# Optimization experiments

Hardware: AMD Instinct MI355X
Metric: run time of the kernel (lower is better)

## Reference

```python
import math
import jax, jax.numpy as jnp
import numpy as np

B, S, HID = 2, 2048, 4096
H, KV = 32, 8
D = HID // H  # 128


def setup_inputs() -> dict:
    key = jax.random.key(0)
    ks = jax.random.split(key, 6)
    std = 0.02
    x = jax.random.normal(ks[0], (B, S, HID), dtype=jnp.float32)
    # causal additive mask, broadcast over batch and heads
    neg = jnp.full((S, S), -1e9, dtype=jnp.float32)
    mask = jnp.triu(neg, k=1)[None, None, :, :]
    q_w = jax.random.normal(ks[1], (HID, HID), dtype=jnp.float32) * std
    k_w = jax.random.normal(ks[2], (KV * D, HID), dtype=jnp.float32) * std
    v_w = jax.random.normal(ks[3], (KV * D, HID), dtype=jnp.float32) * std
    o_w = jax.random.normal(ks[4], (HID, HID), dtype=jnp.float32) * std
    return {
        "x": x, "mask": mask,
        "q_w": q_w, "q_b": jnp.zeros((HID,), jnp.float32),
        "k_w": k_w, "k_b": jnp.zeros((KV * D,), jnp.float32),
        "v_w": v_w, "v_b": jnp.zeros((KV * D,), jnp.float32),
        "o_w": o_w, "o_b": jnp.zeros((HID,), jnp.float32),
    }


def reference(x, mask, q_w, q_b, k_w, k_b, v_w, v_b, o_w, o_b):
    b, s, _ = x.shape
    rep = H // KV
    # projections (torch Linear convention: y = x @ W^T + b)
    q = (x @ q_w.T + q_b).reshape(b, s, H, D)
    k = (x @ k_w.T + k_b).reshape(b, s, KV, D)
    v = (x @ v_w.T + v_b).reshape(b, s, KV, D)
    # GQA kv-head repeat via concat: q head i attends to kv head (i mod KV)
    k = jnp.concatenate([k] * rep, axis=2)  # [b, s, H, D]
    v = jnp.concatenate([v] * rep, axis=2)
    # [b, H, s, D]
    q = q.transpose(0, 2, 1, 3)
    k = k.transpose(0, 2, 1, 3)
    v = v.transpose(0, 2, 1, 3)
    scores = jnp.einsum("bhqd,bhkd->bhqk", q, k) / math.sqrt(D)
    scores = scores + mask
    w = jax.nn.softmax(scores, axis=-1)
    attn = jnp.einsum("bhqk,bhkd->bhqd", w, v)
    attn = attn.transpose(0, 2, 1, 3).reshape(b, s, HID)
    return attn @ o_w.T + o_b
```

## Files before the change

### kernel.cpp

```cpp
#include <hip/hip_runtime.h>
#include <hip/hip_bf16.h>
#include <cstdint>

typedef __attribute__((ext_vector_type(8))) short s8vec;
typedef __attribute__((ext_vector_type(4))) float f4vec;

#define DEV __device__ __forceinline__

constexpr int Bn = 2, Sn = 2048, HIDn = 4096, Hn = 32, KVn = 8, Dn = 128;

typedef const __attribute__((address_space(1))) void gvoid_t;
typedef __attribute__((address_space(3))) void lvoid_t;

DEV void async_ld16(const void* g, void* l) {
  __builtin_amdgcn_global_load_lds((gvoid_t*)g, (lvoid_t*)l, 16, 0, 0);
}

DEV f4vec mfma16(s8vec a, s8vec b, f4vec c) {
  return __builtin_amdgcn_mfma_f32_16x16x32_bf16(a, b, c, 0, 0, 0);
}

__global__ void cvt_all(const float* __restrict__ x, const float* __restrict__ qw,
                        const float* __restrict__ kw, const float* __restrict__ vw,
                        const float* __restrict__ ow,
                        __hip_bfloat16* __restrict__ xb, __hip_bfloat16* __restrict__ qwb,
                        __hip_bfloat16* __restrict__ kwb, __hip_bfloat16* __restrict__ vwb,
                        __hip_bfloat16* __restrict__ owb) {
  const int i = blockIdx.x * 256 + threadIdx.x;
  const float* src; __hip_bfloat16* dst; int off;
  if (i < 4194304)       { src = x;  dst = xb;  off = i; }
  else if (i < 8388608)  { src = qw; dst = qwb; off = i - 4194304; }
  else if (i < 9437184)  { src = kw; dst = kwb; off = i - 8388608; }
  else if (i < 10485760) { src = vw; dst = vwb; off = i - 9437184; }
  else                   { src = ow; dst = owb; off = i - 10485760; }
  float4 f = ((const float4*)src)[off];
  union { __hip_bfloat16 h[4]; uint2 u; } cv;
  cv.h[0] = __float2bfloat16(f.x);
  cv.h[1] = __float2bfloat16(f.y);
  cv.h[2] = __float2bfloat16(f.z);
  cv.h[3] = __float2bfloat16(f.w);
  ((uint2*)dst)[off] = cv.u;
}

template <typename EpiF>
DEV void gemm_bt_body(const __hip_bfloat16* A, const __hip_bfloat16* Bw, int K,
                      long m0, long n0, EpiF epi) {
  __shared__ __hip_bfloat16 As[2][256 * 64];
  __shared__ __hip_bfloat16 Bs[2][256 * 64];
  const int t = threadIdx.x;
  const int w = t >> 6, l = t & 63;
  const int lane15 = l & 15, quad = l >> 4;
  const int wm = (w >> 2) << 7;
  const int wn = (w & 3) << 6;

  f4vec acc[8][4] = {};

  const int srow = w * 8 + (l >> 3);
  const int scol = ((l & 7) ^ (l >> 3)) << 3;
  const __hip_bfloat16* gA = A + (m0 + srow) * (long)K + scol;
  const __hip_bfloat16* gB = Bw + (n0 + srow) * (long)K + scol;
  const long i64K = (long)K << 6;

  auto stage = [&](int buf, int kt) {
    char* la = (char*)As[buf] + (w << 10);
    char* lb = (char*)Bs[buf] + (w << 10);
    const long ko = (long)kt << 6;
#pragma unroll
    for (int i = 0; i < 4; i++) async_ld16(gA + (long)i * i64K + ko, la + i * 8192);
#pragma unroll
    for (int i = 0; i < 4; i++) async_ld16(gB + (long)i * i64K + ko, lb + i * 8192);
  };

  const int arA = (wm + lane15) << 7;
  const int arB = (wn + lane15) << 7;
  const int c0 = (quad << 4) ^ ((lane15 & 7) << 4);
  const int c1 = c0 ^ 64;

  const int NT = K >> 6;

  stage(0, 0);
  stage(1, 1);
  asm volatile("s_waitcnt vmcnt(8)" ::: "memory");
  __builtin_amdgcn_s_barrier();
  __builtin_amdgcn_sched_barrier(0);

  for (int tau = 0; tau < NT; ++tau) {
    const int cur = tau & 1;
    const char* Ab = (const char*)As[cur];
    const char* Bb = (const char*)Bs[cur];
    s8vec af0[8], af1[8], bf0[4], bf1[4];
#pragma unroll
    for (int i = 0; i < 8; i++) {
      af0[i] = *(const s8vec*)(Ab + arA + i * 2048 + c0);
      af1[i] = *(const s8vec*)(Ab + arA + i * 2048 + c1);
    }
#pragma unroll
    for (int j = 0; j < 4; j++) {
      bf0[j] = *(const s8vec*)(Bb + arB + j * 2048 + c0);
      bf1[j] = *(const s8vec*)(Bb + arB + j * 2048 + c1);
    }
    __builtin_amdgcn_s_setprio(1);
#pragma unroll
    for (int i = 0; i < 8; i++)
#pragma unroll
      for (int j = 0; j < 4; j++) acc[i][j] = mfma16(af0[i], bf0[j], acc[i][j]);
    __builtin_amdgcn_s_setprio(0);
    __builtin_amdgcn_sched_barrier(0);
    asm volatile("s_waitcnt lgkmcnt(0)" ::: "memory");
    __builtin_amdgcn_sched_barrier(0);
    __builtin_amdgcn_s_barrier();
    if (tau + 2 < NT) stage(cur, tau + 2);
    __builtin_amdgcn_s_setprio(1);
#pragma unroll
    for (int i = 0; i < 8; i++)
#pragma unroll
      for (int j = 0; j < 4; j++) acc[i][j] = mfma16(af1[i], bf1[j], acc[i][j]);
    __builtin_amdgcn_s_setprio(0);
    if (tau + 1 < NT) {
      if (tau + 2 < NT) asm volatile("s_waitcnt vmcnt(8)" ::: "memory");
      else              asm volatile("s_waitcnt vmcnt(0)" ::: "memory");
      __builtin_amdgcn_s_barrier();
      __builtin_amdgcn_sched_barrier(0);
    }
  }
  epi(acc, wm, wn, lane15, quad);
}

__launch_bounds__(512, 1)
__global__ void gemm_qkv(const __hip_bfloat16* __restrict__ xb,
                         const __hip_bfloat16* __restrict__ qwb,
                         const __hip_bfloat16* __restrict__ kwb,
                         const __hip_bfloat16* __restrict__ vwb,
                         const float* __restrict__ qb, const float* __restrict__ kb,
                         const float* __restrict__ vb,
                         __hip_bfloat16* __restrict__ qh, __hip_bfloat16* __restrict__ kh,
                         __hip_bfloat16* __restrict__ vth) {
  const int bx = blockIdx.x;
  const long m0 = (long)blockIdx.y << 8;
  int mode; long n0;
  const __hip_bfloat16* Bw; const float* bias;
  if (bx < 16)      { mode = 0; Bw = qwb; bias = qb; n0 = (long)bx << 8; }
  else if (bx < 20) { mode = 1; Bw = kwb; bias = kb; n0 = (long)(bx - 16) << 8; }
  else              { mode = 2; Bw = vwb; bias = vb; n0 = (long)(bx - 20) << 8; }

  gemm_bt_body(xb, Bw, 4096, m0, n0,
    [&](f4vec (&acc)[8][4], int wm, int wn, int lane15, int quad) {
      float bv[4];
#pragma unroll
      for (int j = 0; j < 4; j++) bv[j] = bias[n0 + wn + j * 16 + lane15];
#pragma unroll
      for (int i = 0; i < 8; i++)
#pragma unroll
        for (int j = 0; j < 4; j++)
#pragma unroll
          for (int r = 0; r < 4; r++) {
            const long gm = m0 + wm + i * 16 + (quad << 2) + r;
            const long gn = n0 + wn + j * 16 + lane15;
            const float v = acc[i][j][r] + bv[j];
            const long bb = gm >> 11, ss = gm & 2047;
            const long hh = gn >> 7, dd = gn & 127;
            const __hip_bfloat16 hv = __float2bfloat16(v);
            if (mode == 0)
              qh[(((bb * Hn + hh) * Sn + ss) << 7) + dd] = hv;
            else if (mode == 1)
              kh[(((bb * KVn + hh) * Sn + ss) << 7) + dd] = hv;
            else
              vth[((bb * KVn + hh) * Dn + dd) * (long)Sn + ss] = hv;
          }
    });
}

__launch_bounds__(512, 1)
__global__ void gemm_out(const __hip_bfloat16* __restrict__ A,
                         const __hip_bfloat16* __restrict__ Bw,
                         const float* __restrict__ bias, float* __restrict__ Cout) {
  const long m0 = (long)blockIdx.y << 8;
  const long n0 = (long)blockIdx.x << 8;
  gemm_bt_body(A, Bw, 4096, m0, n0,
    [&](f4vec (&acc)[8][4], int wm, int wn, int lane15, int quad) {
      float bv[4];
#pragma unroll
      for (int j = 0; j < 4; j++) bv[j] = bias[n0 + wn + j * 16 + lane15];
#pragma unroll
      for (int i = 0; i < 8; i++)
#pragma unroll
        for (int j = 0; j < 4; j++)
#pragma unroll
          for (int r = 0; r < 4; r++) {
            const long gm = m0 + wm + i * 16 + (quad << 2) + r;
            const long gn = n0 + wn + j * 16 + lane15;
            Cout[gm * HIDn + gn] = acc[i][j][r] + bv[j];
          }
    });
}

__launch_bounds__(256, 2)
__global__ void attn_fused(const __hip_bfloat16* __restrict__ Qh,
                           const __hip_bfloat16* __restrict__ Kh,
                           const __hip_bfloat16* __restrict__ Vt,
                           __hip_bfloat16* __restrict__ Oa) {
  __shared__ __hip_bfloat16 Ks[2][64 * 128];
  __shared__ __hip_bfloat16 Vs[2][128 * 64];
  __shared__ __hip_bfloat16 Ps[4][32 * 64];

  const int pair = blockIdx.x;
  const int h = blockIdx.y;
  const int b = blockIdx.z;
  const int kv = h & 7;

  const int t = threadIdx.x, w = t >> 6, l = t & 63;
  const int lane15 = l & 15, quad = l >> 4;
  const int swz = lane15 & 7;

  const char* KgB = (const char*)(Kh + ((long)(b * KVn + kv)) * Sn * Dn);
  const char* VgB = (const char*)(Vt + ((long)(b * KVn + kv)) * Dn * (long)Sn);

  const int kc = (t & 15) ^ ((t >> 4) & 7);
  const char* kg_base = KgB + (t >> 4) * 256 + kc * 16;
  const int vc = (t & 7) ^ ((t >> 3) & 7);
  const char* vg_base = VgB + (t >> 3) * (size_t)(Sn * 2) + vc * 16;

  const short* Psh = (const short*)Ps[w];
  short* Psw = (short*)Ps[w];
  const float cscale = 0.08838834764831845f * 1.4426950408889634f;
  const float coff = -8.0f * 1.4426950408889634f;

  for (int ph = 0; ph < 2; ph++) {
    const int qt = ph ? (15 - pair) : pair;

    s8vec aq[2][4];
    {
      const short* Qgs = (const short*)(Qh + (((long)(b * Hn + h)) * Sn + qt * 128) * (long)Dn);
#pragma unroll
      for (int i = 0; i < 2; i++)
#pragma unroll
        for (int kk = 0; kk < 4; kk++)
          aq[i][kk] = *(const s8vec*)(Qgs + (w * 32 + i * 16 + lane15) * 128 + kk * 32 + (quad << 3));
    }
    float lsum[2][4] = {};
    f4vec acco[2][8] = {};

    __syncthreads();
    {
      char* lk = (char*)Ks[0] + (w << 10);
      char* lv = (char*)Vs[0] + (w << 10);
#pragma unroll
      for (int i = 0; i < 4; i++) async_ld16(kg_base + i * 4096, lk + i * 4096);
#pragma unroll
      for (int i = 0; i < 4; i++) async_ld16(vg_base + (size_t)i * 32 * Sn * 2, lv + i * 4096);
    }

    const int n_kt = 2 * qt + 2, full_kt = 2 * qt;
    for (int kt = 0; kt < n_kt; kt++) {
      const int cur = kt & 1;
      __syncthreads();
      if (kt + 1 < n_kt) {
        char* lk = (char*)Ks[cur ^ 1] + (w << 10);
        char* lv = (char*)Vs[cur ^ 1] + (w << 10);
        const char* kg = kg_base + (size_t)(kt + 1) * 16384;
        const char* vg = vg_base + (size_t)(kt + 1) * 128;
#pragma unroll
        for (int i = 0; i < 4; i++) async_ld16(kg + i * 4096, lk + i * 4096);
#pragma unroll
        for (int i = 0; i < 4; i++) async_ld16(vg + (size_t)i * 32 * Sn * 2, lv + i * 4096);
      }
      const short* Ksh = (const short*)Ks[cur];
      const short* Vsh = (const short*)Vs[cur];
      const bool need_mask = (kt >= full_kt);

#pragma unroll
      for (int j = 0; j < 4; j++) {
        f4vec as0 = {}, as1 = {};
#pragma unroll
        for (int kk = 0; kk < 4; kk++) {
          const s8vec bk = *(const s8vec*)(Ksh + (j * 16 + lane15) * 128 + (((quad + 4 * kk) ^ swz) << 3));
          as0 = mfma16(aq[0][kk], bk, as0);
          as1 = mfma16(aq[1][kk], bk, as1);
        }
        const int pc = j * 16 + lane15;
        const int kcol = kt * 64 + pc;
#pragma unroll
        for (int i = 0; i < 2; i++) {
#pragma unroll
          for (int r = 0; r < 4; r++) {
            const int pr = i * 16 + (quad << 2) + r;
            float sv = (i ? as1[r] : as0[r]) * cscale + coff;
            if (need_mask) {
              const int qr = qt * 128 + w * 32 + pr;
              if (kcol > qr) sv = -1000000.0f;
            }
            const float p = __builtin_amdgcn_exp2f(sv);
            lsum[i][r] += p;
            Psw[pr * 64 + ((((pc >> 3) ^ (pr & 7)) << 3) | (pc & 7))] =
                __bfloat16_as_short(__float2bfloat16(p));
          }
        }
      }
      asm volatile("s_waitcnt lgkmcnt(0)" ::: "memory");

#pragma unroll
      for (int kk = 0; kk < 2; kk++) {
        s8vec ap[2], bv8[8];
#pragma unroll
        for (int i = 0; i < 2; i++)
          ap[i] = *(const s8vec*)(Psh + (i * 16 + lane15) * 64 + (((quad + 4 * kk) ^ swz) << 3));
#pragma unroll
        for (int j = 0; j < 8; j++)
          bv8[j] = *(const s8vec*)(Vsh + (j * 16 + lane15) * 64 + (((quad + 4 * kk) ^ swz) << 3));
#pragma unroll
        for (int i = 0; i < 2; i++)
#pragma unroll
          for (int j = 0; j < 8; j++)
            acco[i][j] = mfma16(ap[i], bv8[j], acco[i][j]);
      }
    }

#pragma unroll
    for (int i = 0; i < 2; i++)
#pragma unroll
      for (int r = 0; r < 4; r++) {
        float s = lsum[i][r];
#pragma unroll
        for (int d = 1; d < 16; d <<= 1) s += __shfl_xor(s, d);
        lsum[i][r] = 1.0f / s;
      }
#pragma unroll
    for (int i = 0; i < 2; i++) {
#pragma unroll
      for (int r = 0; r < 4; r++) {
        const int row = qt * 128 + w * 32 + i * 16 + (quad << 2) + r;
        const long base = ((long)b * Sn + row) * HIDn + h * Dn;
#pragma unroll
        for (int j = 0; j < 8; j++)
          Oa[base + j * 16 + lane15] = __float2bfloat16(acco[i][j][r] * lsum[i][r]);
      }
    }
  }
}

extern "C" void kernel_launch(void* const* d_in, const int* in_sizes, int n_in,
                              void* d_out, int out_size, void* d_ws, size_t ws_size,
                              hipStream_t stream) {
  const float* x   = (const float*)d_in[0];
  const float* q_w = (const float*)d_in[2];
  const float* q_b = (const float*)d_in[3];
  const float* k_w = (const float*)d_in[4];
  const float* k_b = (const float*)d_in[5];
  const float* v_w = (const float*)d_in[6];
  const float* v_b = (const float*)d_in[7];
  const float* o_w = (const float*)d_in[8];
  const float* o_b = (const float*)d_in[9];

  char* ws = (char*)d_ws;
  size_t off = 0;
  auto nxt = [&](size_t bytes) { char* p = ws + off; off += bytes; return p; };
  __hip_bfloat16* xb  = (__hip_bfloat16*)nxt(33554432);
  __hip_bfloat16* qwb = (__hip_bfloat16*)nxt(33554432);
  __hip_bfloat16* kwb = (__hip_bfloat16*)nxt(8388608);
  __hip_bfloat16* vwb = (__hip_bfloat16*)nxt(8388608);
  __hip_bfloat16* owb = (__hip_bfloat16*)nxt(33554432);
  __hip_bfloat16* qh  = (__hip_bfloat16*)nxt(33554432);
  __hip_bfloat16* kh  = (__hip_bfloat16*)nxt(8388608);
  __hip_bfloat16* vth = (__hip_bfloat16*)nxt(8388608);
  __hip_bfloat16* at  = (__hip_bfloat16*)nxt(33554432);
  (void)ws_size; (void)in_sizes; (void)n_in; (void)out_size;

  cvt_all<<<57344, 256, 0, stream>>>(x, q_w, k_w, v_w, o_w, xb, qwb, kwb, vwb, owb);
  gemm_qkv<<<dim3(24, 16), 512, 0, stream>>>(xb, qwb, kwb, vwb, q_b, k_b, v_b, qh, kh, vth);
  attn_fused<<<dim3(8, 32, 2), 256, 0, stream>>>(qh, kh, vth, at);
  gemm_out<<<dim3(16, 16), 512, 0, stream>>>(at, owb, o_b, (float*)d_out);
}
```

Before: 719.6 us.

## Restructure GEMM mainloop into 4-stage half-K LDS ring with staggered A/B prefetch

The shared GEMM body switches from a double-buffered 64-wide K tile to a four-slot ring of 32-wide K sub-tiles for A and B, with a new XOR swizzle and thread-to-row mapping for the async global-to-LDS loads. Each K step is split into four MFMA phases, each loading only half the A fragments and reusing B fragments. A and B prefetches are interleaved between phases with tuned vmcnt waits. The aim is to lower register pressure from fragment arrays and to overlap memory traffic with compute more finely. The cost is many more barriers per iteration and fragile wait-count bookkeeping.

```diff
diff --git a/kernel.cpp b/kernel.cpp
--- a/kernel.cpp
+++ b/kernel.cpp
@@ -45,8 +45,8 @@
 template <typename EpiF>
 DEV void gemm_bt_body(const __hip_bfloat16* A, const __hip_bfloat16* Bw, int K,
                       long m0, long n0, EpiF epi) {
-  __shared__ __hip_bfloat16 As[2][256 * 64];
-  __shared__ __hip_bfloat16 Bs[2][256 * 64];
+  __shared__ __hip_bfloat16 As[4][256 * 32];
+  __shared__ __hip_bfloat16 Bs[4][256 * 32];
   const int t = threadIdx.x;
   const int w = t >> 6, l = t & 63;
   const int lane15 = l & 15, quad = l >> 4;
@@ -55,72 +55,110 @@
 
   f4vec acc[8][4] = {};
 
-  const int srow = w * 8 + (l >> 3);
-  const int scol = ((l & 7) ^ (l >> 3)) << 3;
+  const int srow = t >> 2;
+  const int scol = ((t & 3) ^ ((srow >> 1) & 3)) << 3;
   const __hip_bfloat16* gA = A + (m0 + srow) * (long)K + scol;
   const __hip_bfloat16* gB = Bw + (n0 + srow) * (long)K + scol;
-  const long i64K = (long)K << 6;
-
-  auto stage = [&](int buf, int kt) {
-    char* la = (char*)As[buf] + (w << 10);
-    char* lb = (char*)Bs[buf] + (w << 10);
-    const long ko = (long)kt << 6;
-#pragma unroll
-    for (int i = 0; i < 4; i++) async_ld16(gA + (long)i * i64K + ko, la + i * 8192);
-#pragma unroll
-    for (int i = 0; i < 4; i++) async_ld16(gB + (long)i * i64K + ko, lb + i * 8192);
+  const long half128 = (long)128 * K;
+
+  auto stageA = [&](int n) {
+    char* d = (char*)As + ((n & 3) << 14) + t * 16;
+    const __hip_bfloat16* g = gA + (long)n * 32;
+    async_ld16(g, d);
+    async_ld16(g + half128, d + 8192);
   };
-
-  const int arA = (wm + lane15) << 7;
-  const int arB = (wn + lane15) << 7;
-  const int c0 = (quad << 4) ^ ((lane15 & 7) << 4);
-  const int c1 = c0 ^ 64;
+  auto stageB = [&](int n) {
+    char* d = (char*)Bs + ((n & 3) << 14) + t * 16;
+    const __hip_bfloat16* g = gB + (long)n * 32;
+    async_ld16(g, d);
+    async_ld16(g + half128, d + 8192);
+  };
+
+  const int rswz = (quad ^ ((lane15 >> 1) & 3)) << 4;
+  const int aoff = (wm + lane15) * 64 + rswz;
+  const int boff = (wn + lane15) * 64 + rswz;
+
+  auto ldA = [&](const char* base, int i) { return *(const s8vec*)(base + aoff + i * 1024); };
+  auto ldB = [&](const char* base, int j) { return *(const s8vec*)(base + boff + j * 1024); };
 
   const int NT = K >> 6;
 
-  stage(0, 0);
-  stage(1, 1);
-  asm volatile("s_waitcnt vmcnt(8)" ::: "memory");
+  stageA(0); stageB(0); stageA(1); stageB(1); stageA(2); stageB(2); stageB(3);
+  asm volatile("s_waitcnt vmcnt(10)" ::: "memory");
   __builtin_amdgcn_s_barrier();
-  __builtin_amdgcn_sched_barrier(0);
-
-  for (int tau = 0; tau < NT; ++tau) {
-    const int cur = tau & 1;
-    const char* Ab = (const char*)As[cur];
-    const char* Bb = (const char*)Bs[cur];
-    s8vec af0[8], af1[8], bf0[4], bf1[4];
-#pragma unroll
-    for (int i = 0; i < 8; i++) {
-      af0[i] = *(const s8vec*)(Ab + arA + i * 2048 + c0);
-      af1[i] = *(const s8vec*)(Ab + arA + i * 2048 + c1);
-    }
-#pragma unroll
-    for (int j = 0; j < 4; j++) {
-      bf0[j] = *(const s8vec*)(Bb + arB + j * 2048 + c0);
-      bf1[j] = *(const s8vec*)(Bb + arB + j * 2048 + c1);
-    }
-    __builtin_amdgcn_s_setprio(1);
-#pragma unroll
-    for (int i = 0; i < 8; i++)
-#pragma unroll
-      for (int j = 0; j < 4; j++) acc[i][j] = mfma16(af0[i], bf0[j], acc[i][j]);
-    __builtin_amdgcn_s_setprio(0);
-    __builtin_amdgcn_sched_barrier(0);
+
+  for (int kt = 0; kt < NT; ++kt) {
+    const char* Ak0 = (const char*)As + (((2 * kt) & 3) << 14);
+    const char* Bk0 = (const char*)Bs + (((2 * kt) & 3) << 14);
+    const char* Ak1 = (const char*)As + (((2 * kt + 1) & 3) << 14);
+    const char* Bk1 = (const char*)Bs + (((2 * kt + 1) & 3) << 14);
+    s8vec a4[4], b4[4];
+
+#pragma unroll
+    for (int i = 0; i < 4; i++) a4[i] = ldA(Ak0, i);
+#pragma unroll
+    for (int j = 0; j < 4; j++) b4[j] = ldB(Bk0, j);
+    if (kt + 1 < NT) stageA(2 * kt + 3);
+    __builtin_amdgcn_s_barrier();
     asm volatile("s_waitcnt lgkmcnt(0)" ::: "memory");
     __builtin_amdgcn_sched_barrier(0);
-    __builtin_amdgcn_s_barrier();
-    if (tau + 2 < NT) stage(cur, tau + 2);
     __builtin_amdgcn_s_setprio(1);
 #pragma unroll
-    for (int i = 0; i < 8; i++)
-#pragma unroll
-      for (int j = 0; j < 4; j++) acc[i][j] = mfma16(af1[i], bf1[j], acc[i][j]);
+    for (int i = 0; i < 4; i++)
+#pragma unroll
+      for (int j = 0; j < 4; j++) acc[i][j] = mfma16(a4[i], b4[j], acc[i][j]);
     __builtin_amdgcn_s_setprio(0);
-    if (tau + 1 < NT) {
-      if (tau + 2 < NT) asm volatile("s_waitcnt vmcnt(8)" ::: "memory");
-      else              asm volatile("s_waitcnt vmcnt(0)" ::: "memory");
+    __builtin_amdgcn_s_barrier();
+
+#pragma unroll
+    for (int i = 0; i < 4; i++) a4[i] = ldA(Ak0, 4 + i);
+    if (kt + 2 < NT) stageB(2 * kt + 4);
+    __builtin_amdgcn_s_barrier();
+    asm volatile("s_waitcnt lgkmcnt(0)" ::: "memory");
+    __builtin_amdgcn_sched_barrier(0);
+    __builtin_amdgcn_s_setprio(1);
+#pragma unroll
+    for (int i = 0; i < 4; i++)
+#pragma unroll
+      for (int j = 0; j < 4; j++) acc[4 + i][j] = mfma16(a4[i], b4[j], acc[4 + i][j]);
+    __builtin_amdgcn_s_setprio(0);
+    if (kt < NT - 2)       asm volatile("s_waitcnt vmcnt(10)" ::: "memory");
+    else if (kt == NT - 2) asm volatile("s_waitcnt vmcnt(8)" ::: "memory");
+    else                   asm volatile("s_waitcnt vmcnt(0)" ::: "memory");
+    __builtin_amdgcn_s_barrier();
+
+#pragma unroll
+    for (int i = 0; i < 4; i++) a4[i] = ldA(Ak1, i);
+#pragma unroll
+    for (int j = 0; j < 4; j++) b4[j] = ldB(Bk1, j);
+    if (kt + 2 < NT) stageA(2 * kt + 4);
+    __builtin_amdgcn_s_barrier();
+    asm volatile("s_waitcnt lgkmcnt(0)" ::: "memory");
+    __builtin_amdgcn_sched_barrier(0);
+    __builtin_amdgcn_s_setprio(1);
+#pragma unroll
+    for (int i = 0; i < 4; i++)
+#pragma unroll
+      for (int j = 0; j < 4; j++) acc[i][j] = mfma16(a4[i], b4[j], acc[i][j]);
+    __builtin_amdgcn_s_setprio(0);
+    __builtin_amdgcn_s_barrier();
+
+#pragma unroll
+    for (int i = 0; i < 4; i++) a4[i] = ldA(Ak1, 4 + i);
+    if (kt + 2 < NT) stageB(2 * kt + 5);
+    __builtin_amdgcn_s_barrier();
+    asm volatile("s_waitcnt lgkmcnt(0)" ::: "memory");
+    __builtin_amdgcn_sched_barrier(0);
+    __builtin_amdgcn_s_setprio(1);
+#pragma unroll
+    for (int i = 0; i < 4; i++)
+#pragma unroll
+      for (int j = 0; j < 4; j++) acc[4 + i][j] = mfma16(a4[i], b4[j], acc[4 + i][j]);
+    __builtin_amdgcn_s_setprio(0);
+    if (kt + 1 < NT) {
+      if (kt < NT - 2) asm volatile("s_waitcnt vmcnt(10)" ::: "memory");
+      else             asm volatile("s_waitcnt vmcnt(4)" ::: "memory");
       __builtin_amdgcn_s_barrier();
-      __builtin_amdgcn_sched_barrier(0);
     }
   }
   epi(acc, wm, wn, lane15, quad);
```

Measured after the change: 755.8 us. 5.0% more time.
